# Optimization experiments

Hardware: AMD Instinct MI355X
Metric: run time of the kernel (lower is better)

## Reference

```python
import jax, jax.numpy as jnp
import numpy as np

V, E, H, L, S, T = 100000, 256, 512, 50000, 512, 64


def setup_inputs() -> dict:
    key = jax.random.key(0)
    ks = jax.random.split(key, 14)
    s = 0.02
    return {
        "encoder_outputs": jax.random.normal(ks[0], (1, S, H), jnp.float32),
        "enc_h0": jax.random.normal(ks[1], (1, 1, H), jnp.float32),
        "enc_c0": jax.random.normal(ks[2], (1, 1, H), jnp.float32),
        "emb_table": jax.random.normal(ks[3], (V, E), jnp.float32) * s,
        "W_attn": jax.random.normal(ks[4], (H, E), jnp.float32) * s,
        "b_attn": jnp.zeros((H,), jnp.float32),
        "W_ih": jax.random.normal(ks[5], (4 * H, H), jnp.float32) * s,
        "W_hh": jax.random.normal(ks[6], (4 * H, H), jnp.float32) * s,
        "b_ih": jnp.zeros((4 * H,), jnp.float32),
        "b_hh": jnp.zeros((4 * H,), jnp.float32),
        "W_out": jax.random.normal(ks[7], (L, H), jnp.float32) * s,
        "b_out": jnp.zeros((L,), jnp.float32),
        "word_inputs": jax.random.randint(ks[8], (T,), 0, V),
        "labels": jax.random.randint(ks[9], (T,), 0, L),
    }


def reference(encoder_outputs, enc_h0, enc_c0, emb_table, W_attn, b_attn,
              W_ih, W_hh, b_ih, b_hh, W_out, b_out, word_inputs, labels):
    # batch == 1 throughout (matches forward_train); dropout is identity (eval).
    enc = encoder_outputs[0]          # [S, H]
    h0 = enc_h0[0, 0]                 # [H]  (bidirect hidden already flattened to 1x1xH)
    c0 = enc_c0[0, 0]                 # [H]

    def step(carry, xs):
        h, c = carry
        widx, label = xs
        e = emb_table[widx]                               # [E]   embedding lookup
        q = W_attn @ e + b_attn                           # [H]   attn projection (Linear)
        alphas = jax.nn.softmax(enc @ q)                  # [S]   bmm + softmax
        ctx = alphas @ enc                                # [H]   bmm -> context
        # single-step LSTM (PyTorch gate order: i, f, g, o)
        gates = W_ih @ ctx + b_ih + W_hh @ h + b_hh       # [4H]
        i, f, g, o = jnp.split(gates, 4)
        i = jax.nn.sigmoid(i); f = jax.nn.sigmoid(f)
        g = jnp.tanh(g);       o = jax.nn.sigmoid(o)
        c2 = f * c + i * g
        h2 = o * jnp.tanh(c2)
        logits = W_out @ h2 + b_out                       # [L]   hidden2tag
        ls = jax.nn.log_softmax(logits)
        # NLLLoss(ignore_index=0, reduction='sum')
        step_loss = jnp.where(label == 0, jnp.float32(0.0), -ls[label])
        return (h2, c2), step_loss

    (_, _), losses = jax.lax.scan(step, (h0, c0),
                                  (word_inputs, labels))
    return jnp.sum(losses)
```

## Files before the change

kernel.cpp:

```cpp
#include <hip/hip_runtime.h>
#include <hip/hip_bf16.h>

#define V_ 100000
#define E_ 256
#define H_ 512
#define L_ 50000
#define S_ 512
#define T_ 64
#define NB_ 782
#define NBP_ 784
#define NWG_ 32

typedef short bf16x8 __attribute__((ext_vector_type(8)));
typedef float f32x4 __attribute__((ext_vector_type(4)));

__device__ __forceinline__ float sigm(float x){ return 1.0f/(1.0f+__expf(-x)); }
__device__ __forceinline__ float tanh_fast(float x){
    x = fminf(fmaxf(x, -15.f), 15.f);
    float e = __expf(2.f * x);
    return __fdividef(e - 1.f, e + 1.f);
}
__device__ __forceinline__ unsigned bf16rne(float x){
    unsigned u = __float_as_uint(x);
    return (u + 0x7fffu + ((u >> 16) & 1u)) >> 16;
}
__device__ __forceinline__ float bcast(float v, int l){
    return __uint_as_float(__builtin_amdgcn_readlane(__float_as_uint(v), l));
}

__global__ __launch_bounds__(256) void k_attn(
    const float* __restrict__ enc, const float* __restrict__ emb,
    const float* __restrict__ W_attn, const float* __restrict__ b_attn,
    const int* __restrict__ word_inputs, float* __restrict__ ctx_out)
{
    __shared__ float e_l[E_];
    __shared__ float q_l[H_];
    __shared__ float sc[S_];
    __shared__ float red[8];
    const int t = blockIdx.x, tid = threadIdx.x;
    const int widx = word_inputs[t];

    e_l[tid] = emb[(long)widx * E_ + tid];
    __syncthreads();

    for (int rr = 0; rr < 2; ++rr) {
        int r = tid + rr * 256;
        const float4* wrow = (const float4*)(W_attn + r * E_);
        const float4* ev = (const float4*)e_l;
        float acc = b_attn[r];
        #pragma unroll 8
        for (int j = 0; j < E_ / 4; ++j) {
            float4 w = wrow[j], e4 = ev[j];
            acc += w.x*e4.x + w.y*e4.y + w.z*e4.z + w.w*e4.w;
        }
        q_l[r] = acc;
    }
    __syncthreads();

    for (int rr = 0; rr < 2; ++rr) {
        int s = tid + rr * 256;
        const float4* er = (const float4*)(enc + s * H_);
        const float4* qv = (const float4*)q_l;
        float acc = 0.f;
        #pragma unroll 8
        for (int j = 0; j < H_ / 4; ++j) {
            float4 a = er[j], b = qv[j];
            acc += a.x*b.x + a.y*b.y + a.z*b.z + a.w*b.w;
        }
        sc[s] = acc;
    }
    __syncthreads();

    float m = fmaxf(sc[tid], sc[tid + 256]);
    for (int off = 32; off; off >>= 1) m = fmaxf(m, __shfl_down(m, off));
    if ((tid & 63) == 0) red[tid >> 6] = m;
    __syncthreads();
    if (tid == 0) red[4] = fmaxf(fmaxf(red[0], red[1]), fmaxf(red[2], red[3]));
    __syncthreads();
    m = red[4];
    float e0 = __expf(sc[tid] - m), e1 = __expf(sc[tid + 256] - m);
    sc[tid] = e0; sc[tid + 256] = e1;
    float ssum = e0 + e1;
    for (int off = 32; off; off >>= 1) ssum += __shfl_down(ssum, off);
    if ((tid & 63) == 0) red[tid >> 6] = ssum;
    __syncthreads();
    if (tid == 0) red[5] = red[0] + red[1] + red[2] + red[3];
    __syncthreads();
    float inv = 1.0f / red[5];

    for (int rr = 0; rr < 2; ++rr) {
        int h = tid + rr * 256;
        float acc = 0.f;
        #pragma unroll 4
        for (int s = 0; s < S_; ++s) acc += sc[s] * enc[s * H_ + h];
        ctx_out[t * H_ + h] = acc * inv;
    }
}

__global__ __launch_bounds__(256) void k_gatepre(
    const float* __restrict__ ctx, const float* __restrict__ W_ih,
    const float* __restrict__ b_ih, const float* __restrict__ b_hh,
    float* __restrict__ A_pre)
{
    __shared__ float ctx_t[H_ * 65];
    __shared__ float w_l[8 * H_];
    const int tid = threadIdx.x;
    const int r0 = blockIdx.x * 8;

    for (int i = 0; i < 32; ++i) {
        int p = tid + i * 256;
        int t = p >> 7, k4 = p & 127;
        float4 v = ((const float4*)ctx)[p];
        ctx_t[(k4*4+0)*65 + t] = v.x;
        ctx_t[(k4*4+1)*65 + t] = v.y;
        ctx_t[(k4*4+2)*65 + t] = v.z;
        ctx_t[(k4*4+3)*65 + t] = v.w;
    }
    for (int i = 0; i < 4; ++i) {
        int p = tid + i * 256;
        int row = p >> 7, k4 = p & 127;
        float4 v = ((const float4*)W_ih)[(r0 + row) * (H_/4) + k4];
        float* dst = &w_l[row * H_ + k4 * 4];
        dst[0]=v.x; dst[1]=v.y; dst[2]=v.z; dst[3]=v.w;
    }
    __syncthreads();

    const int t = tid & 63, half = tid >> 6;
    const float* w0 = &w_l[(half*2+0) * H_];
    const float* w1 = &w_l[(half*2+1) * H_];
    float acc0 = 0.f, acc1 = 0.f;
    #pragma unroll 4
    for (int k = 0; k < H_; ++k) {
        float cv = ctx_t[k * 65 + t];
        acc0 += w0[k] * cv;
        acc1 += w1[k] * cv;
    }
    int ra = r0 + half * 2, rb = ra + 1;
    A_pre[t * 2048 + ra] = acc0 + b_ih[ra] + b_hh[ra];
    A_pre[t * 2048 + rb] = acc1 + b_ih[rb] + b_hh[rb];
}

#define ST(i, val) asm volatile("v_accvgpr_write_b32 %0, %1" : "=a"(g##i) : "v"(val));
#define STQ(q,i0,i1,i2,i3) { float4 v_ = wsrc[q]; ST(i0,v_.x) ST(i1,v_.y) ST(i2,v_.z) ST(i3,v_.w) }
#define RD1(i) float wv##i; asm volatile("v_accvgpr_read_b32 %0, %1" : "=v"(wv##i) : "a"(g##i));
#define RD4(i0,i1,i2,i3) RD1(i0) RD1(i1) RD1(i2) RD1(i3)
#define FMA4(i0,i1,i2,i3) \
    a0 += wv##i0 * bcast(hv, i0); a1 += wv##i1 * bcast(hv, i1); \
    a2 += wv##i2 * bcast(hv, i2); a3 += wv##i3 * bcast(hv, i3);

__global__ __launch_bounds__(512, 1) void k_lstm(
    const float* __restrict__ W_hh, const float* __restrict__ A_pre,
    const float* __restrict__ h0, const float* __restrict__ c0,
    float* __restrict__ h_buf)
{
    const int tid = threadIdx.x, wg = blockIdx.x;

    __shared__ float A_l[T_ * 64];
    __shared__ float red[2][8][64];

    const int base = wg * 16;
    const int lane = tid & 63;
    const int ks   = tid >> 6;
    const int G = ((lane >> 4) << 9) + base + (lane & 15);

    float g0,g1,g2,g3,g4,g5,g6,g7,g8,g9,g10,g11,g12,g13,g14,g15;
    float g16,g17,g18,g19,g20,g21,g22,g23,g24,g25,g26,g27,g28,g29,g30,g31;
    float g32,g33,g34,g35,g36,g37,g38,g39,g40,g41,g42,g43,g44,g45,g46,g47;
    float g48,g49,g50,g51,g52,g53,g54,g55,g56,g57,g58,g59,g60,g61,g62,g63;
    {
        const float4* wsrc = (const float4*)(W_hh + (long)G * H_ + ks * 64);
        STQ(0,0,1,2,3)     STQ(1,4,5,6,7)     STQ(2,8,9,10,11)   STQ(3,12,13,14,15)
        STQ(4,16,17,18,19) STQ(5,20,21,22,23) STQ(6,24,25,26,27) STQ(7,28,29,30,31)
        STQ(8,32,33,34,35) STQ(9,36,37,38,39) STQ(10,40,41,42,43)STQ(11,44,45,46,47)
        STQ(12,48,49,50,51)STQ(13,52,53,54,55)STQ(14,56,57,58,59)STQ(15,60,61,62,63)
    }

    for (int i = 0; i < 8; ++i) {
        int p = tid + i * 512;
        int tt = p >> 6, rr = p & 63;
        A_l[p] = A_pre[tt * 2048 + ((rr >> 4) << 9) + base + (rr & 15)];
    }
    float c_reg = 0.f;
    if (tid < 16) c_reg = c0[base + tid];
    __syncthreads();

    const unsigned SENT = 0xFFFFFFFFu;

    for (int t = 0; t < T_; ++t) {
        RD4(0,1,2,3)     RD4(4,5,6,7)     RD4(8,9,10,11)   RD4(12,13,14,15)
        RD4(16,17,18,19) RD4(20,21,22,23) RD4(24,25,26,27) RD4(28,29,30,31)
        RD4(32,33,34,35) RD4(36,37,38,39) RD4(40,41,42,43) RD4(44,45,46,47)
        RD4(48,49,50,51) RD4(52,53,54,55) RD4(56,57,58,59) RD4(60,61,62,63)
        __builtin_amdgcn_sched_barrier(0);

        float hv;
        if (t == 0) {
            hv = h0[ks * 64 + lane];
        } else {
            const unsigned* hb = (const unsigned*)h_buf + (t - 1) * H_ + ks * 64;
            unsigned u = __hip_atomic_load(hb + lane, __ATOMIC_RELAXED,
                                           __HIP_MEMORY_SCOPE_AGENT);
            while (u == SENT) {
                __builtin_amdgcn_s_sleep(1);
                u = __hip_atomic_load(hb + lane, __ATOMIC_RELAXED,
                                      __HIP_MEMORY_SCOPE_AGENT);
            }
            hv = __uint_as_float(u);
        }

        float a0 = 0.f, a1 = 0.f, a2 = 0.f, a3 = 0.f;
        FMA4(0,1,2,3)     FMA4(4,5,6,7)     FMA4(8,9,10,11)   FMA4(12,13,14,15)
        FMA4(16,17,18,19) FMA4(20,21,22,23) FMA4(24,25,26,27) FMA4(28,29,30,31)
        FMA4(32,33,34,35) FMA4(36,37,38,39) FMA4(40,41,42,43) FMA4(44,45,46,47)
        FMA4(48,49,50,51) FMA4(52,53,54,55) FMA4(56,57,58,59) FMA4(60,61,62,63)
        red[t & 1][ks][lane] = (a0 + a1) + (a2 + a3);
        __syncthreads();

        if (ks == 0) {
            float s = A_l[t * 64 + lane];
            #pragma unroll
            for (int k2 = 0; k2 < 8; ++k2) s += red[t & 1][k2][lane];
            float gf_ = __shfl_down(s, 16);
            float gg_ = __shfl_down(s, 32);
            float go_ = __shfl_down(s, 48);
            if (lane < 16) {
                float gi = sigm(s);
                float gf = sigm(gf_);
                float gg = tanh_fast(gg_);
                float go = sigm(go_);
                float c2 = gf * c_reg + gi * gg;
                c_reg = c2;
                float h2 = go * tanh_fast(c2);
                __hip_atomic_store((unsigned*)h_buf + t * H_ + base + lane,
                                   __float_as_uint(h2),
                                   __ATOMIC_RELAXED, __HIP_MEMORY_SCOPE_AGENT);
            }
        }
    }
}

__global__ __launch_bounds__(256) void k_out(
    const float* __restrict__ W_out, const float* __restrict__ b_out,
    const float* __restrict__ h_buf, const int* __restrict__ labels,
    float* __restrict__ pm, float* __restrict__ ps, float* __restrict__ ll)
{
    __shared__ __align__(16) unsigned char smem[65536];
    const int tid = threadIdx.x;
    const int r0 = blockIdx.x * 64;
    const int lane = tid & 63, w = tid >> 6;
    const int g = lane >> 4, li = lane & 15;

    for (int i = 0; i < 32; ++i) {
        int p = tid + i * 256;
        int t = p >> 7, k4 = p & 127;
        float4 v = ((const float4*)h_buf)[p];
        unsigned p01 = bf16rne(v.x) | (bf16rne(v.y) << 16);
        unsigned p23 = bf16rne(v.z) | (bf16rne(v.w) << 16);
        unsigned byte = (unsigned)(t * 1024 + k4 * 8) ^ ((unsigned)(t & 7) << 4);
        *(uint2*)(smem + byte) = make_uint2(p01, p23);
    }

    f32x4 acc0 = {0.f,0.f,0.f,0.f}, acc1 = {0.f,0.f,0.f,0.f};
    f32x4 acc2 = {0.f,0.f,0.f,0.f}, acc3 = {0.f,0.f,0.f,0.f};
    __syncthreads();

    int rrow = r0 + w * 16 + li;
    int rw = rrow < L_ ? rrow : (L_ - 1);
    const float* ap = W_out + (long)rw * H_ + g * 8;

    #pragma unroll
    for (int kk = 0; kk < 16; ++kk) {
        float4 va = *(const float4*)(ap + kk * 32);
        float4 vb = *(const float4*)(ap + kk * 32 + 4);
        union { unsigned u[4]; bf16x8 v; } A;
        A.u[0] = bf16rne(va.x) | (bf16rne(va.y) << 16);
        A.u[1] = bf16rne(va.z) | (bf16rne(va.w) << 16);
        A.u[2] = bf16rne(vb.x) | (bf16rne(vb.y) << 16);
        A.u[3] = bf16rne(vb.z) | (bf16rne(vb.w) << 16);

        #pragma unroll
        for (int nt = 0; nt < 4; ++nt) {
            int t = nt * 16 + li;
            unsigned byte = (unsigned)(t * 1024 + kk * 64 + g * 16)
                          ^ ((unsigned)(t & 7) << 4);
            bf16x8 B = *(const bf16x8*)(smem + byte);
            f32x4* accp = (nt == 0) ? &acc0 : (nt == 1) ? &acc1
                        : (nt == 2) ? &acc2 : &acc3;
            *accp = __builtin_amdgcn_mfma_f32_16x16x32_bf16(A.v, B, *accp, 0, 0, 0);
        }
    }
    __syncthreads();

    float* lg   = (float*)smem;
    float* redb = (float*)(smem + 64 * 65 * 4);
    float* gmax = redb + 256;

    #pragma unroll
    for (int nt = 0; nt < 4; ++nt) {
        const f32x4 a = (nt == 0) ? acc0 : (nt == 1) ? acc1
                      : (nt == 2) ? acc2 : acc3;
        int t = nt * 16 + li;
        #pragma unroll
        for (int q = 0; q < 4; ++q) {
            int rloc = w * 16 + g * 4 + q;
            int r = r0 + rloc;
            float v = -1e30f;
            if (r < L_) v = a[q] + b_out[r];
            lg[rloc * 65 + t] = v;
        }
    }
    __syncthreads();

    const int t = tid & 63, part = tid >> 6;
    float m = -1e30f;
    #pragma unroll
    for (int r16 = 0; r16 < 16; ++r16)
        m = fmaxf(m, lg[(part*16 + r16)*65 + t]);
    redb[part*64 + t] = m;
    __syncthreads();
    if (part == 0)
        gmax[t] = fmaxf(fmaxf(redb[t], redb[64+t]), fmaxf(redb[128+t], redb[192+t]));
    __syncthreads();
    float gm = gmax[t];
    float s = 0.f;
    #pragma unroll
    for (int r16 = 0; r16 < 16; ++r16)
        s += __expf(lg[(part*16 + r16)*65 + t] - gm);
    __syncthreads();
    redb[part*64 + t] = s;
    __syncthreads();
    if (part == 0) {
        pm[t * NBP_ + blockIdx.x] = gm;
        ps[t * NBP_ + blockIdx.x] = redb[t] + redb[64+t] + redb[128+t] + redb[192+t];
        int lb = labels[t];
        if (lb >= r0 && lb < r0 + 64) ll[t] = lg[(lb - r0)*65 + t];
    }
}

__global__ __launch_bounds__(256) void k_final(
    const float* __restrict__ pm, const float* __restrict__ ps,
    const float* __restrict__ ll, const int* __restrict__ labels,
    float* __restrict__ out)
{
    __shared__ float rbuf[8];
    const int t = blockIdx.x, tid = threadIdx.x;
    float m = -1e30f;
    for (int b = tid; b < NB_; b += 256) m = fmaxf(m, pm[t * NBP_ + b]);
    for (int off = 32; off; off >>= 1) m = fmaxf(m, __shfl_down(m, off));
    if ((tid & 63) == 0) rbuf[tid >> 6] = m;
    __syncthreads();
    if (tid == 0) rbuf[4] = fmaxf(fmaxf(rbuf[0], rbuf[1]), fmaxf(rbuf[2], rbuf[3]));
    __syncthreads();
    float M = rbuf[4];
    __syncthreads();
    float s = 0.f;
    for (int b = tid; b < NB_; b += 256)
        s += ps[t * NBP_ + b] * __expf(pm[t * NBP_ + b] - M);
    for (int off = 32; off; off >>= 1) s += __shfl_down(s, off);
    if ((tid & 63) == 0) rbuf[tid >> 6] = s;
    __syncthreads();
    if (tid == 0) {
        float S = rbuf[0] + rbuf[1] + rbuf[2] + rbuf[3];
        int lb = labels[t];
        if (lb != 0) {
            float loss = -(ll[t] - M - __logf(S));
            atomicAdd(out, loss);
        }
    }
}

extern "C" void kernel_launch(void* const* d_in, const int* in_sizes, int n_in,
                              void* d_out, int out_size, void* d_ws, size_t ws_size,
                              hipStream_t stream)
{
    (void)in_sizes; (void)n_in; (void)out_size; (void)ws_size;
    const float* enc    = (const float*)d_in[0];
    const float* h0     = (const float*)d_in[1];
    const float* c0     = (const float*)d_in[2];
    const float* emb    = (const float*)d_in[3];
    const float* W_attn = (const float*)d_in[4];
    const float* b_attn = (const float*)d_in[5];
    const float* W_ih   = (const float*)d_in[6];
    const float* W_hh   = (const float*)d_in[7];
    const float* b_ih   = (const float*)d_in[8];
    const float* b_hh   = (const float*)d_in[9];
    const float* W_out  = (const float*)d_in[10];
    const float* b_out  = (const float*)d_in[11];
    const int* widx     = (const int*)d_in[12];
    const int* labels   = (const int*)d_in[13];
    float* out = (float*)d_out;

    char* ws = (char*)d_ws;
    float* ctx   = (float*)(ws + 0);
    float* A_pre = (float*)(ws + 131072);
    float* h_buf = (float*)(ws + 655360);
    float* pm    = (float*)(ws + 786688);
    float* ps    = (float*)(ws + 987392);
    float* ll    = (float*)(ws + 1188096);

    hipMemsetAsync(h_buf, 0xFF, T_ * H_ * sizeof(float), stream);
    hipMemsetAsync(out, 0, sizeof(float), stream);

    k_attn<<<T_, 256, 0, stream>>>(enc, emb, W_attn, b_attn, widx, ctx);
    k_gatepre<<<256, 256, 0, stream>>>(ctx, W_ih, b_ih, b_hh, A_pre);
    k_lstm<<<NWG_, 512, 0, stream>>>(W_hh, A_pre, h0, c0, h_buf);
    k_out<<<NB_, 256, 0, stream>>>(W_out, b_out, h_buf, labels, pm, ps, ll);
    k_final<<<T_, 256, 0, stream>>>(pm, ps, ll, labels, out);
}
```

Before: 240.1 us.

## Convert W_out to bf16 on idle CUs during the LSTM recurrence

Extra workgroups are added to the latency-bound LSTM launch. They convert W_out from fp32 to bf16 into the workspace while the 32 recurrence workgroups run, and the LSTM also writes h in bf16. A new output kernel reads the pre-converted bf16 weights and h directly from global memory, which halves the bytes it streams and removes the per-tile conversion and shared-memory staging. The risk is that the converter blocks contend for bandwidth and CUs with the recurrence, and the path only runs when the workspace holds about 52 MB.

```diff
diff --git a/kernel.cpp b/kernel.cpp
--- a/kernel.cpp
+++ b/kernel.cpp
@@ -10,6 +10,7 @@
 #define NB_ 782
 #define NBP_ 784
 #define NWG_ 32
+#define NCV_ 224
 
 typedef short bf16x8 __attribute__((ext_vector_type(8)));
 typedef float f32x4 __attribute__((ext_vector_type(4)));
@@ -151,9 +152,26 @@
 __global__ __launch_bounds__(512, 1) void k_lstm(
     const float* __restrict__ W_hh, const float* __restrict__ A_pre,
     const float* __restrict__ h0, const float* __restrict__ c0,
-    float* __restrict__ h_buf)
-{
-    const int tid = threadIdx.x, wg = blockIdx.x;
+    float* __restrict__ h_buf, unsigned short* __restrict__ h_bf,
+    unsigned short* __restrict__ w_bf, const float* __restrict__ W_out)
+{
+    const int tid = threadIdx.x, bid = blockIdx.x;
+
+    if (bid >= NWG_) {
+        const int cid = bid - NWG_;
+        const long total4 = (long)L_ * H_ / 4;
+        const long stride = (long)NCV_ * 512;
+        const float4* src = (const float4*)W_out;
+        uint2* dst = (uint2*)w_bf;
+        for (long i = (long)cid * 512 + tid; i < total4; i += stride) {
+            float4 v = src[i];
+            unsigned lo = bf16rne(v.x) | (bf16rne(v.y) << 16);
+            unsigned hi = bf16rne(v.z) | (bf16rne(v.w) << 16);
+            dst[i] = make_uint2(lo, hi);
+        }
+        return;
+    }
+    const int wg = bid;
 
     __shared__ float A_l[T_ * 64];
     __shared__ float red[2][8][64];
@@ -234,66 +252,45 @@
                 __hip_atomic_store((unsigned*)h_buf + t * H_ + base + lane,
                                    __float_as_uint(h2),
                                    __ATOMIC_RELAXED, __HIP_MEMORY_SCOPE_AGENT);
+                h_bf[t * H_ + base + lane] = (unsigned short)bf16rne(h2);
             }
         }
     }
 }
 
-__global__ __launch_bounds__(256) void k_out(
-    const float* __restrict__ W_out, const float* __restrict__ b_out,
-    const float* __restrict__ h_buf, const int* __restrict__ labels,
+__global__ __launch_bounds__(256) void k_out_bf(
+    const unsigned short* __restrict__ w_bf, const float* __restrict__ b_out,
+    const unsigned short* __restrict__ h_bf, const int* __restrict__ labels,
     float* __restrict__ pm, float* __restrict__ ps, float* __restrict__ ll)
 {
-    __shared__ __align__(16) unsigned char smem[65536];
+    __shared__ float lg[64 * 65];
+    __shared__ float redb[256];
+    __shared__ float gmax[64];
     const int tid = threadIdx.x;
     const int r0 = blockIdx.x * 64;
     const int lane = tid & 63, w = tid >> 6;
     const int g = lane >> 4, li = lane & 15;
 
-    for (int i = 0; i < 32; ++i) {
-        int p = tid + i * 256;
-        int t = p >> 7, k4 = p & 127;
-        float4 v = ((const float4*)h_buf)[p];
-        unsigned p01 = bf16rne(v.x) | (bf16rne(v.y) << 16);
-        unsigned p23 = bf16rne(v.z) | (bf16rne(v.w) << 16);
-        unsigned byte = (unsigned)(t * 1024 + k4 * 8) ^ ((unsigned)(t & 7) << 4);
-        *(uint2*)(smem + byte) = make_uint2(p01, p23);
-    }
-
     f32x4 acc0 = {0.f,0.f,0.f,0.f}, acc1 = {0.f,0.f,0.f,0.f};
     f32x4 acc2 = {0.f,0.f,0.f,0.f}, acc3 = {0.f,0.f,0.f,0.f};
-    __syncthreads();
 
     int rrow = r0 + w * 16 + li;
     int rw = rrow < L_ ? rrow : (L_ - 1);
-    const float* ap = W_out + (long)rw * H_ + g * 8;
+    const bf16x8* ap = (const bf16x8*)(w_bf + (long)rw * H_);
+    const bf16x8* hp = (const bf16x8*)h_bf;
 
     #pragma unroll
     for (int kk = 0; kk < 16; ++kk) {
-        float4 va = *(const float4*)(ap + kk * 32);
-        float4 vb = *(const float4*)(ap + kk * 32 + 4);
-        union { unsigned u[4]; bf16x8 v; } A;
-        A.u[0] = bf16rne(va.x) | (bf16rne(va.y) << 16);
-        A.u[1] = bf16rne(va.z) | (bf16rne(va.w) << 16);
-        A.u[2] = bf16rne(vb.x) | (bf16rne(vb.y) << 16);
-        A.u[3] = bf16rne(vb.z) | (bf16rne(vb.w) << 16);
-
-        #pragma unroll
-        for (int nt = 0; nt < 4; ++nt) {
-            int t = nt * 16 + li;
-            unsigned byte = (unsigned)(t * 1024 + kk * 64 + g * 16)
-                          ^ ((unsigned)(t & 7) << 4);
-            bf16x8 B = *(const bf16x8*)(smem + byte);
-            f32x4* accp = (nt == 0) ? &acc0 : (nt == 1) ? &acc1
-                        : (nt == 2) ? &acc2 : &acc3;
-            *accp = __builtin_amdgcn_mfma_f32_16x16x32_bf16(A.v, B, *accp, 0, 0, 0);
-        }
-    }
-    __syncthreads();
-
-    float* lg   = (float*)smem;
-    float* redb = (float*)(smem + 64 * 65 * 4);
-    float* gmax = redb + 256;
+        bf16x8 A = ap[kk * 4 + g];
+        bf16x8 B0 = hp[(0*16 + li) * 64 + kk*4 + g];
+        bf16x8 B1 = hp[(1*16 + li) * 64 + kk*4 + g];
+        bf16x8 B2 = hp[(2*16 + li) * 64 + kk*4 + g];
+        bf16x8 B3 = hp[(3*16 + li) * 64 + kk*4 + g];
+        acc0 = __builtin_amdgcn_mfma_f32_16x16x32_bf16(A, B0, acc0, 0, 0, 0);
+        acc1 = __builtin_amdgcn_mfma_f32_16x16x32_bf16(A, B1, acc1, 0, 0, 0);
+        acc2 = __builtin_amdgcn_mfma_f32_16x16x32_bf16(A, B2, acc2, 0, 0, 0);
+        acc3 = __builtin_amdgcn_mfma_f32_16x16x32_bf16(A, B3, acc3, 0, 0, 0);
+    }
 
     #pragma unroll
     for (int nt = 0; nt < 4; ++nt) {
@@ -337,6 +334,104 @@
     }
 }
 
+__global__ __launch_bounds__(256) void k_out(
+    const float* __restrict__ W_out, const float* __restrict__ b_out,
+    const float* __restrict__ h_buf, const int* __restrict__ labels,
+    float* __restrict__ pm, float* __restrict__ ps, float* __restrict__ ll)
+{
+    __shared__ __align__(16) unsigned char smem[65536];
+    const int tid = threadIdx.x;
+    const int r0 = blockIdx.x * 64;
+    const int lane = tid & 63, w = tid >> 6;
+    const int g = lane >> 4, li = lane & 15;
+
+    for (int i = 0; i < 32; ++i) {
+        int p = tid + i * 256;
+        int t = p >> 7, k4 = p & 127;
+        float4 v = ((const float4*)h_buf)[p];
+        unsigned p01 = bf16rne(v.x) | (bf16rne(v.y) << 16);
+        unsigned p23 = bf16rne(v.z) | (bf16rne(v.w) << 16);
+        unsigned byte = (unsigned)(t * 1024 + k4 * 8) ^ ((unsigned)(t & 7) << 4);
+        *(uint2*)(smem + byte) = make_uint2(p01, p23);
+    }
+
+    f32x4 acc0 = {0.f,0.f,0.f,0.f}, acc1 = {0.f,0.f,0.f,0.f};
+    f32x4 acc2 = {0.f,0.f,0.f,0.f}, acc3 = {0.f,0.f,0.f,0.f};
+    __syncthreads();
+
+    int rrow = r0 + w * 16 + li;
+    int rw = rrow < L_ ? rrow : (L_ - 1);
+    const float* ap = W_out + (long)rw * H_ + g * 8;
+
+    #pragma unroll
+    for (int kk = 0; kk < 16; ++kk) {
+        float4 va = *(const float4*)(ap + kk * 32);
+        float4 vb = *(const float4*)(ap + kk * 32 + 4);
+        union { unsigned u[4]; bf16x8 v; } A;
+        A.u[0] = bf16rne(va.x) | (bf16rne(va.y) << 16);
+        A.u[1] = bf16rne(va.z) | (bf16rne(va.w) << 16);
+        A.u[2] = bf16rne(vb.x) | (bf16rne(vb.y) << 16);
+        A.u[3] = bf16rne(vb.z) | (bf16rne(vb.w) << 16);
+
+        #pragma unroll
+        for (int nt = 0; nt < 4; ++nt) {
+            int t = nt * 16 + li;
+            unsigned byte = (unsigned)(t * 1024 + kk * 64 + g * 16)
+                          ^ ((unsigned)(t & 7) << 4);
+            bf16x8 B = *(const bf16x8*)(smem + byte);
+            f32x4* accp = (nt == 0) ? &acc0 : (nt == 1) ? &acc1
+                        : (nt == 2) ? &acc2 : &acc3;
+            *accp = __builtin_amdgcn_mfma_f32_16x16x32_bf16(A.v, B, *accp, 0, 0, 0);
+        }
+    }
+    __syncthreads();
+
+    float* lg   = (float*)smem;
+    float* redb = (float*)(smem + 64 * 65 * 4);
+    float* gmax = redb + 256;
+
+    #pragma unroll
+    for (int nt = 0; nt < 4; ++nt) {
+        const f32x4 a = (nt == 0) ? acc0 : (nt == 1) ? acc1
+                      : (nt == 2) ? acc2 : acc3;
+        int t = nt * 16 + li;
+        #pragma unroll
+        for (int q = 0; q < 4; ++q) {
+            int rloc = w * 16 + g * 4 + q;
+            int r = r0 + rloc;
+            float v = -1e30f;
+            if (r < L_) v = a[q] + b_out[r];
+            lg[rloc * 65 + t] = v;
+        }
+    }
+    __syncthreads();
+
+    const int t = tid & 63, part = tid >> 6;
+    float m = -1e30f;
+    #pragma unroll
+    for (int r16 = 0; r16 < 16; ++r16)
+        m = fmaxf(m, lg[(part*16 + r16)*65 + t]);
+    redb[part*64 + t] = m;
+    __syncthreads();
+    if (part == 0)
+        gmax[t] = fmaxf(fmaxf(redb[t], redb[64+t]), fmaxf(redb[128+t], redb[192+t]));
+    __syncthreads();
+    float gm = gmax[t];
+    float s = 0.f;
+    #pragma unroll
+    for (int r16 = 0; r16 < 16; ++r16)
+        s += __expf(lg[(part*16 + r16)*65 + t] - gm);
+    __syncthreads();
+    redb[part*64 + t] = s;
+    __syncthreads();
+    if (part == 0) {
+        pm[t * NBP_ + blockIdx.x] = gm;
+        ps[t * NBP_ + blockIdx.x] = redb[t] + redb[64+t] + redb[128+t] + redb[192+t];
+        int lb = labels[t];
+        if (lb >= r0 && lb < r0 + 64) ll[t] = lg[(lb - r0)*65 + t];
+    }
+}
+
 __global__ __launch_bounds__(256) void k_final(
     const float* __restrict__ pm, const float* __restrict__ ps,
     const float* __restrict__ ll, const int* __restrict__ labels,
@@ -373,7 +468,7 @@
                               void* d_out, int out_size, void* d_ws, size_t ws_size,
                               hipStream_t stream)
 {
-    (void)in_sizes; (void)n_in; (void)out_size; (void)ws_size;
+    (void)in_sizes; (void)n_in; (void)out_size;
     const float* enc    = (const float*)d_in[0];
     const float* h0     = (const float*)d_in[1];
     const float* c0     = (const float*)d_in[2];
@@ -391,19 +486,30 @@
     float* out = (float*)d_out;
 
     char* ws = (char*)d_ws;
-    float* ctx   = (float*)(ws + 0);
-    float* A_pre = (float*)(ws + 131072);
-    float* h_buf = (float*)(ws + 655360);
-    float* pm    = (float*)(ws + 786688);
-    float* ps    = (float*)(ws + 987392);
-    float* ll    = (float*)(ws + 1188096);
+    float* ctx            = (float*)(ws + 0);
+    float* A_pre          = (float*)(ws + 131072);
+    float* h_buf          = (float*)(ws + 655360);
+    float* pm             = (float*)(ws + 786688);
+    float* ps             = (float*)(ws + 987392);
+    float* ll             = (float*)(ws + 1188096);
+    unsigned short* h_bf  = (unsigned short*)(ws + 1188352);
+    unsigned short* w_bf  = (unsigned short*)(ws + 1253888);
+
+    const bool fast = ws_size >= (size_t)52453888;
 
     hipMemsetAsync(h_buf, 0xFF, T_ * H_ * sizeof(float), stream);
     hipMemsetAsync(out, 0, sizeof(float), stream);
 
     k_attn<<<T_, 256, 0, stream>>>(enc, emb, W_attn, b_attn, widx, ctx);
     k_gatepre<<<256, 256, 0, stream>>>(ctx, W_ih, b_ih, b_hh, A_pre);
-    k_lstm<<<NWG_, 512, 0, stream>>>(W_hh, A_pre, h0, c0, h_buf);
-    k_out<<<NB_, 256, 0, stream>>>(W_out, b_out, h_buf, labels, pm, ps, ll);
+    if (fast) {
+        k_lstm<<<NWG_ + NCV_, 512, 0, stream>>>(W_hh, A_pre, h0, c0,
+                                                h_buf, h_bf, w_bf, W_out);
+        k_out_bf<<<NB_, 256, 0, stream>>>(w_bf, b_out, h_bf, labels, pm, ps, ll);
+    } else {
+        k_lstm<<<NWG_, 512, 0, stream>>>(W_hh, A_pre, h0, c0,
+                                         h_buf, h_bf, h_bf , W_out);
+        k_out<<<NB_, 256, 0, stream>>>(W_out, b_out, h_buf, labels, pm, ps, ll);
+    }
     k_final<<<T_, 256, 0, stream>>>(pm, ps, ll, labels, out);
 }
```

New measurement: 260.2 us. 1.08x slower.

## Fuse attention and input-gate projection into the persistent LSTM kernel

Applied to the files above, without the earlier changes.

Merges the attention kernel and the W_ih gate-precompute kernel into the persistent LSTM kernel. Each of the 32 workgroups computes attention context for two timesteps and publishes it to global memory through sentinel-checked atomics. It then holds its W_ih slice in AGPRs and computes its own gate pre-activations before running the recurrence. This removes two kernel launches and the A_pre round trip through global memory. In exchange it doubles AGPR pressure, concentrates attention work on only 32 workgroups, and makes every workgroup spin-wait on contexts produced by the others.

```diff
diff --git a/kernel.cpp b/kernel.cpp
--- a/kernel.cpp
+++ b/kernel.cpp
@@ -28,145 +28,53 @@
     return __uint_as_float(__builtin_amdgcn_readlane(__float_as_uint(v), l));
 }
 
-__global__ __launch_bounds__(256) void k_attn(
-    const float* __restrict__ enc, const float* __restrict__ emb,
-    const float* __restrict__ W_attn, const float* __restrict__ b_attn,
-    const int* __restrict__ word_inputs, float* __restrict__ ctx_out)
-{
-    __shared__ float e_l[E_];
-    __shared__ float q_l[H_];
-    __shared__ float sc[S_];
-    __shared__ float red[8];
-    const int t = blockIdx.x, tid = threadIdx.x;
-    const int widx = word_inputs[t];
-
-    e_l[tid] = emb[(long)widx * E_ + tid];
-    __syncthreads();
-
-    for (int rr = 0; rr < 2; ++rr) {
-        int r = tid + rr * 256;
-        const float4* wrow = (const float4*)(W_attn + r * E_);
-        const float4* ev = (const float4*)e_l;
-        float acc = b_attn[r];
-        #pragma unroll 8
-        for (int j = 0; j < E_ / 4; ++j) {
-            float4 w = wrow[j], e4 = ev[j];
-            acc += w.x*e4.x + w.y*e4.y + w.z*e4.z + w.w*e4.w;
-        }
-        q_l[r] = acc;
-    }
-    __syncthreads();
-
-    for (int rr = 0; rr < 2; ++rr) {
-        int s = tid + rr * 256;
-        const float4* er = (const float4*)(enc + s * H_);
-        const float4* qv = (const float4*)q_l;
-        float acc = 0.f;
-        #pragma unroll 8
-        for (int j = 0; j < H_ / 4; ++j) {
-            float4 a = er[j], b = qv[j];
-            acc += a.x*b.x + a.y*b.y + a.z*b.z + a.w*b.w;
-        }
-        sc[s] = acc;
-    }
-    __syncthreads();
-
-    float m = fmaxf(sc[tid], sc[tid + 256]);
-    for (int off = 32; off; off >>= 1) m = fmaxf(m, __shfl_down(m, off));
-    if ((tid & 63) == 0) red[tid >> 6] = m;
-    __syncthreads();
-    if (tid == 0) red[4] = fmaxf(fmaxf(red[0], red[1]), fmaxf(red[2], red[3]));
-    __syncthreads();
-    m = red[4];
-    float e0 = __expf(sc[tid] - m), e1 = __expf(sc[tid + 256] - m);
-    sc[tid] = e0; sc[tid + 256] = e1;
-    float ssum = e0 + e1;
-    for (int off = 32; off; off >>= 1) ssum += __shfl_down(ssum, off);
-    if ((tid & 63) == 0) red[tid >> 6] = ssum;
-    __syncthreads();
-    if (tid == 0) red[5] = red[0] + red[1] + red[2] + red[3];
-    __syncthreads();
-    float inv = 1.0f / red[5];
-
-    for (int rr = 0; rr < 2; ++rr) {
-        int h = tid + rr * 256;
-        float acc = 0.f;
-        #pragma unroll 4
-        for (int s = 0; s < S_; ++s) acc += sc[s] * enc[s * H_ + h];
-        ctx_out[t * H_ + h] = acc * inv;
-    }
-}
-
-__global__ __launch_bounds__(256) void k_gatepre(
-    const float* __restrict__ ctx, const float* __restrict__ W_ih,
-    const float* __restrict__ b_ih, const float* __restrict__ b_hh,
-    float* __restrict__ A_pre)
-{
-    __shared__ float ctx_t[H_ * 65];
-    __shared__ float w_l[8 * H_];
-    const int tid = threadIdx.x;
-    const int r0 = blockIdx.x * 8;
-
-    for (int i = 0; i < 32; ++i) {
-        int p = tid + i * 256;
-        int t = p >> 7, k4 = p & 127;
-        float4 v = ((const float4*)ctx)[p];
-        ctx_t[(k4*4+0)*65 + t] = v.x;
-        ctx_t[(k4*4+1)*65 + t] = v.y;
-        ctx_t[(k4*4+2)*65 + t] = v.z;
-        ctx_t[(k4*4+3)*65 + t] = v.w;
-    }
-    for (int i = 0; i < 4; ++i) {
-        int p = tid + i * 256;
-        int row = p >> 7, k4 = p & 127;
-        float4 v = ((const float4*)W_ih)[(r0 + row) * (H_/4) + k4];
-        float* dst = &w_l[row * H_ + k4 * 4];
-        dst[0]=v.x; dst[1]=v.y; dst[2]=v.z; dst[3]=v.w;
-    }
-    __syncthreads();
-
-    const int t = tid & 63, half = tid >> 6;
-    const float* w0 = &w_l[(half*2+0) * H_];
-    const float* w1 = &w_l[(half*2+1) * H_];
-    float acc0 = 0.f, acc1 = 0.f;
-    #pragma unroll 4
-    for (int k = 0; k < H_; ++k) {
-        float cv = ctx_t[k * 65 + t];
-        acc0 += w0[k] * cv;
-        acc1 += w1[k] * cv;
-    }
-    int ra = r0 + half * 2, rb = ra + 1;
-    A_pre[t * 2048 + ra] = acc0 + b_ih[ra] + b_hh[ra];
-    A_pre[t * 2048 + rb] = acc1 + b_ih[rb] + b_hh[rb];
-}
-
 #define ST(i, val) asm volatile("v_accvgpr_write_b32 %0, %1" : "=a"(g##i) : "v"(val));
 #define STQ(q,i0,i1,i2,i3) { float4 v_ = wsrc[q]; ST(i0,v_.x) ST(i1,v_.y) ST(i2,v_.z) ST(i3,v_.w) }
+#define STJ(i, val) asm volatile("v_accvgpr_write_b32 %0, %1" : "=a"(j##i) : "v"(val));
+#define STJQ(q,i0,i1,i2,i3) { float4 v_ = wsrc2[q]; STJ(i0,v_.x) STJ(i1,v_.y) STJ(i2,v_.z) STJ(i3,v_.w) }
 #define RD1(i) float wv##i; asm volatile("v_accvgpr_read_b32 %0, %1" : "=v"(wv##i) : "a"(g##i));
 #define RD4(i0,i1,i2,i3) RD1(i0) RD1(i1) RD1(i2) RD1(i3)
 #define FMA4(i0,i1,i2,i3) \
     a0 += wv##i0 * bcast(hv, i0); a1 += wv##i1 * bcast(hv, i1); \
     a2 += wv##i2 * bcast(hv, i2); a3 += wv##i3 * bcast(hv, i3);
-
-__global__ __launch_bounds__(512, 1) void k_lstm(
-    const float* __restrict__ W_hh, const float* __restrict__ A_pre,
+#define MJ4(i0,i1,i2,i3) { float w0_,w1_,w2_,w3_; \
+  asm volatile("v_accvgpr_read_b32 %0, %1" : "=v"(w0_) : "a"(j##i0)); \
+  asm volatile("v_accvgpr_read_b32 %0, %1" : "=v"(w1_) : "a"(j##i1)); \
+  asm volatile("v_accvgpr_read_b32 %0, %1" : "=v"(w2_) : "a"(j##i2)); \
+  asm volatile("v_accvgpr_read_b32 %0, %1" : "=v"(w3_) : "a"(j##i3)); \
+  a0 += w0_ * bcast(cv, i0); a1 += w1_ * bcast(cv, i1); \
+  a2 += w2_ * bcast(cv, i2); a3 += w3_ * bcast(cv, i3); }
+
+__global__ __launch_bounds__(512, 1) void k_fused(
+    const float* __restrict__ enc, const float* __restrict__ emb,
+    const float* __restrict__ W_attn, const float* __restrict__ b_attn,
+    const int* __restrict__ word_inputs,
+    const float* __restrict__ W_ih, const float* __restrict__ b_ih,
+    const float* __restrict__ b_hh, const float* __restrict__ W_hh,
     const float* __restrict__ h0, const float* __restrict__ c0,
-    float* __restrict__ h_buf)
+    float* __restrict__ ctx_g, float* __restrict__ h_buf)
 {
-    const int tid = threadIdx.x, wg = blockIdx.x;
-
     __shared__ float A_l[T_ * 64];
     __shared__ float red[2][8][64];
-
-    const int base = wg * 16;
+    __shared__ float e_l2[512];
+    __shared__ float q_l2[1024];
+    __shared__ float sc2[1024];
+    __shared__ float red8[16];
+
+    const int tid = threadIdx.x, wg = blockIdx.x;
     const int lane = tid & 63;
     const int ks   = tid >> 6;
+    const int base = wg * 16;
     const int G = ((lane >> 4) << 9) + base + (lane & 15);
 
     float g0,g1,g2,g3,g4,g5,g6,g7,g8,g9,g10,g11,g12,g13,g14,g15;
     float g16,g17,g18,g19,g20,g21,g22,g23,g24,g25,g26,g27,g28,g29,g30,g31;
     float g32,g33,g34,g35,g36,g37,g38,g39,g40,g41,g42,g43,g44,g45,g46,g47;
     float g48,g49,g50,g51,g52,g53,g54,g55,g56,g57,g58,g59,g60,g61,g62,g63;
+    float j0,j1,j2,j3,j4,j5,j6,j7,j8,j9,j10,j11,j12,j13,j14,j15;
+    float j16,j17,j18,j19,j20,j21,j22,j23,j24,j25,j26,j27,j28,j29,j30,j31;
+    float j32,j33,j34,j35,j36,j37,j38,j39,j40,j41,j42,j43,j44,j45,j46,j47;
+    float j48,j49,j50,j51,j52,j53,j54,j55,j56,j57,j58,j59,j60,j61,j62,j63;
     {
         const float4* wsrc = (const float4*)(W_hh + (long)G * H_ + ks * 64);
         STQ(0,0,1,2,3)     STQ(1,4,5,6,7)     STQ(2,8,9,10,11)   STQ(3,12,13,14,15)
@@ -174,17 +82,123 @@
         STQ(8,32,33,34,35) STQ(9,36,37,38,39) STQ(10,40,41,42,43)STQ(11,44,45,46,47)
         STQ(12,48,49,50,51)STQ(13,52,53,54,55)STQ(14,56,57,58,59)STQ(15,60,61,62,63)
     }
-
-    for (int i = 0; i < 8; ++i) {
-        int p = tid + i * 512;
-        int tt = p >> 6, rr = p & 63;
-        A_l[p] = A_pre[tt * 2048 + ((rr >> 4) << 9) + base + (rr & 15)];
-    }
+    {
+        const float4* wsrc2 = (const float4*)(W_ih + (long)G * H_ + ks * 64);
+        STJQ(0,0,1,2,3)     STJQ(1,4,5,6,7)     STJQ(2,8,9,10,11)   STJQ(3,12,13,14,15)
+        STJQ(4,16,17,18,19) STJQ(5,20,21,22,23) STJQ(6,24,25,26,27) STJQ(7,28,29,30,31)
+        STJQ(8,32,33,34,35) STJQ(9,36,37,38,39) STJQ(10,40,41,42,43)STJQ(11,44,45,46,47)
+        STJQ(12,48,49,50,51)STJQ(13,52,53,54,55)STJQ(14,56,57,58,59)STJQ(15,60,61,62,63)
+    }
+
     float c_reg = 0.f;
     if (tid < 16) c_reg = c0[base + tid];
-    __syncthreads();
+    float bb = 0.f;
+    if (tid < 64) bb = b_ih[G] + b_hh[G];
 
     const unsigned SENT = 0xFFFFFFFFu;
+
+    {
+        const int t0 = wg * 2, t1 = wg * 2 + 1;
+        const int w0i = word_inputs[t0], w1i = word_inputs[t1];
+        if (tid < 256) e_l2[tid] = emb[(long)w0i * E_ + tid];
+        else           e_l2[tid] = emb[(long)w1i * E_ + (tid - 256)];
+        __syncthreads();
+
+        {
+            const float4* wrow = (const float4*)(W_attn + tid * E_);
+            const float4* e0p = (const float4*)e_l2;
+            const float4* e1p = (const float4*)(e_l2 + 256);
+            float acc0 = b_attn[tid], acc1 = acc0;
+            #pragma unroll 8
+            for (int j2 = 0; j2 < E_ / 4; ++j2) {
+                float4 w = wrow[j2], a = e0p[j2], b = e1p[j2];
+                acc0 += w.x*a.x + w.y*a.y + w.z*a.z + w.w*a.w;
+                acc1 += w.x*b.x + w.y*b.y + w.z*b.z + w.w*b.w;
+            }
+            q_l2[tid] = acc0; q_l2[512 + tid] = acc1;
+        }
+        __syncthreads();
+
+        float acc0 = 0.f, acc1 = 0.f;
+        {
+            const float4* er = (const float4*)(enc + tid * H_);
+            const float4* q0p = (const float4*)q_l2;
+            const float4* q1p = (const float4*)(q_l2 + 512);
+            #pragma unroll 8
+            for (int j2 = 0; j2 < H_ / 4; ++j2) {
+                float4 e = er[j2], a = q0p[j2], b = q1p[j2];
+                acc0 += e.x*a.x + e.y*a.y + e.z*a.z + e.w*a.w;
+                acc1 += e.x*b.x + e.y*b.y + e.z*b.z + e.w*b.w;
+            }
+        }
+        float m0 = acc0, m1 = acc1;
+        for (int off = 32; off; off >>= 1) {
+            m0 = fmaxf(m0, __shfl_down(m0, off));
+            m1 = fmaxf(m1, __shfl_down(m1, off));
+        }
+        if (lane == 0) { red8[ks] = m0; red8[8 + ks] = m1; }
+        __syncthreads();
+        float M0 = red8[0], M1 = red8[8];
+        #pragma unroll
+        for (int i2 = 1; i2 < 8; ++i2) {
+            M0 = fmaxf(M0, red8[i2]); M1 = fmaxf(M1, red8[8 + i2]);
+        }
+        float e0v = __expf(acc0 - M0), e1v = __expf(acc1 - M1);
+        sc2[tid] = e0v; sc2[512 + tid] = e1v;
+        float s0 = e0v, s1 = e1v;
+        for (int off = 32; off; off >>= 1) {
+            s0 += __shfl_down(s0, off);
+            s1 += __shfl_down(s1, off);
+        }
+        __syncthreads();
+        if (lane == 0) { red8[ks] = s0; red8[8 + ks] = s1; }
+        __syncthreads();
+        float S0 = 0.f, S1 = 0.f;
+        #pragma unroll
+        for (int i2 = 0; i2 < 8; ++i2) { S0 += red8[i2]; S1 += red8[8 + i2]; }
+        float inv0 = 1.f / S0, inv1 = 1.f / S1;
+
+        float c0a = 0.f, c1a = 0.f;
+        #pragma unroll 4
+        for (int s = 0; s < S_; ++s) {
+            float ev = enc[s * H_ + tid];
+            c0a += sc2[s] * ev;
+            c1a += sc2[512 + s] * ev;
+        }
+        c0a *= inv0; c1a *= inv1;
+        __hip_atomic_store((unsigned*)ctx_g + t0 * H_ + tid, __float_as_uint(c0a),
+                           __ATOMIC_RELAXED, __HIP_MEMORY_SCOPE_AGENT);
+        __hip_atomic_store((unsigned*)ctx_g + t1 * H_ + tid, __float_as_uint(c1a),
+                           __ATOMIC_RELAXED, __HIP_MEMORY_SCOPE_AGENT);
+    }
+
+    for (int t = 0; t < T_; ++t) {
+        float cv;
+        {
+            const unsigned* cb = (const unsigned*)ctx_g + t * H_ + ks * 64;
+            unsigned u = __hip_atomic_load(cb + lane, __ATOMIC_RELAXED,
+                                           __HIP_MEMORY_SCOPE_AGENT);
+            while (u == SENT) {
+                __builtin_amdgcn_s_sleep(1);
+                u = __hip_atomic_load(cb + lane, __ATOMIC_RELAXED,
+                                      __HIP_MEMORY_SCOPE_AGENT);
+            }
+            cv = __uint_as_float(u);
+        }
+        float a0 = 0.f, a1 = 0.f, a2 = 0.f, a3 = 0.f;
+        MJ4(0,1,2,3)     MJ4(4,5,6,7)     MJ4(8,9,10,11)   MJ4(12,13,14,15)
+        MJ4(16,17,18,19) MJ4(20,21,22,23) MJ4(24,25,26,27) MJ4(28,29,30,31)
+        MJ4(32,33,34,35) MJ4(36,37,38,39) MJ4(40,41,42,43) MJ4(44,45,46,47)
+        MJ4(48,49,50,51) MJ4(52,53,54,55) MJ4(56,57,58,59) MJ4(60,61,62,63)
+        red[t & 1][ks][lane] = (a0 + a1) + (a2 + a3);
+        __syncthreads();
+        if (ks == 0) {
+            float s = bb;
+            #pragma unroll
+            for (int k2 = 0; k2 < 8; ++k2) s += red[t & 1][k2][lane];
+            A_l[t * 64 + lane] = s;
+        }
+    }
 
     for (int t = 0; t < T_; ++t) {
         RD4(0,1,2,3)     RD4(4,5,6,7)     RD4(8,9,10,11)   RD4(12,13,14,15)
@@ -391,19 +405,18 @@
     float* out = (float*)d_out;
 
     char* ws = (char*)d_ws;
-    float* ctx   = (float*)(ws + 0);
-    float* A_pre = (float*)(ws + 131072);
-    float* h_buf = (float*)(ws + 655360);
-    float* pm    = (float*)(ws + 786688);
-    float* ps    = (float*)(ws + 987392);
-    float* ll    = (float*)(ws + 1188096);
-
-    hipMemsetAsync(h_buf, 0xFF, T_ * H_ * sizeof(float), stream);
+    float* h_buf = (float*)(ws + 0);
+    float* ctx_g = (float*)(ws + 131072);
+    float* pm    = (float*)(ws + 262144);
+    float* ps    = (float*)(ws + 462848);
+    float* ll    = (float*)(ws + 663552);
+
+    hipMemsetAsync(h_buf, 0xFF, 2 * T_ * H_ * sizeof(float), stream);
     hipMemsetAsync(out, 0, sizeof(float), stream);
 
-    k_attn<<<T_, 256, 0, stream>>>(enc, emb, W_attn, b_attn, widx, ctx);
-    k_gatepre<<<256, 256, 0, stream>>>(ctx, W_ih, b_ih, b_hh, A_pre);
-    k_lstm<<<NWG_, 512, 0, stream>>>(W_hh, A_pre, h0, c0, h_buf);
+    k_fused<<<NWG_, 512, 0, stream>>>(enc, emb, W_attn, b_attn, widx,
+                                      W_ih, b_ih, b_hh, W_hh, h0, c0,
+                                      ctx_g, h_buf);
     k_out<<<NB_, 256, 0, stream>>>(W_out, b_out, h_buf, labels, pm, ps, ll);
     k_final<<<T_, 256, 0, stream>>>(pm, ps, ll, labels, out);
 }
```

Result: slower. 270.9 us (+12.8%).

## Rewrite attention kernel with wave-cooperative coalesced row dot products

Applied to the files above, without the earlier changes.

The attention kernel moves from one-thread-per-row dot products to one-wave-per-row dot products. Each lane reads a contiguous float4 slice of the W_attn or encoder row, and the partial sums are combined with xor shuffles. The aim is to replace strided, uncoalesced per-thread row reads with coalesced loads. The block size also doubles to 512 so the context reduction needs one column per thread. The cost is added shuffle reductions for every row.

```diff
diff --git a/kernel.cpp b/kernel.cpp
--- a/kernel.cpp
+++ b/kernel.cpp
@@ -28,7 +28,7 @@
     return __uint_as_float(__builtin_amdgcn_readlane(__float_as_uint(v), l));
 }
 
-__global__ __launch_bounds__(256) void k_attn(
+__global__ __launch_bounds__(512) void k_attn2(
     const float* __restrict__ enc, const float* __restrict__ emb,
     const float* __restrict__ W_attn, const float* __restrict__ b_attn,
     const int* __restrict__ word_inputs, float* __restrict__ ctx_out)
@@ -36,65 +36,73 @@
     __shared__ float e_l[E_];
     __shared__ float q_l[H_];
     __shared__ float sc[S_];
-    __shared__ float red[8];
+    __shared__ float red8[8];
     const int t = blockIdx.x, tid = threadIdx.x;
+    const int lane = tid & 63, wv = tid >> 6;
     const int widx = word_inputs[t];
 
-    e_l[tid] = emb[(long)widx * E_ + tid];
-    __syncthreads();
-
-    for (int rr = 0; rr < 2; ++rr) {
-        int r = tid + rr * 256;
-        const float4* wrow = (const float4*)(W_attn + r * E_);
-        const float4* ev = (const float4*)e_l;
-        float acc = b_attn[r];
-        #pragma unroll 8
-        for (int j = 0; j < E_ / 4; ++j) {
-            float4 w = wrow[j], e4 = ev[j];
-            acc += w.x*e4.x + w.y*e4.y + w.z*e4.z + w.w*e4.w;
-        }
-        q_l[r] = acc;
-    }
-    __syncthreads();
-
-    for (int rr = 0; rr < 2; ++rr) {
-        int s = tid + rr * 256;
-        const float4* er = (const float4*)(enc + s * H_);
-        const float4* qv = (const float4*)q_l;
-        float acc = 0.f;
-        #pragma unroll 8
-        for (int j = 0; j < H_ / 4; ++j) {
-            float4 a = er[j], b = qv[j];
-            acc += a.x*b.x + a.y*b.y + a.z*b.z + a.w*b.w;
-        }
-        sc[s] = acc;
-    }
-    __syncthreads();
-
-    float m = fmaxf(sc[tid], sc[tid + 256]);
-    for (int off = 32; off; off >>= 1) m = fmaxf(m, __shfl_down(m, off));
-    if ((tid & 63) == 0) red[tid >> 6] = m;
-    __syncthreads();
-    if (tid == 0) red[4] = fmaxf(fmaxf(red[0], red[1]), fmaxf(red[2], red[3]));
-    __syncthreads();
-    m = red[4];
-    float e0 = __expf(sc[tid] - m), e1 = __expf(sc[tid + 256] - m);
-    sc[tid] = e0; sc[tid + 256] = e1;
-    float ssum = e0 + e1;
-    for (int off = 32; off; off >>= 1) ssum += __shfl_down(ssum, off);
-    if ((tid & 63) == 0) red[tid >> 6] = ssum;
-    __syncthreads();
-    if (tid == 0) red[5] = red[0] + red[1] + red[2] + red[3];
-    __syncthreads();
-    float inv = 1.0f / red[5];
-
-    for (int rr = 0; rr < 2; ++rr) {
-        int h = tid + rr * 256;
-        float acc = 0.f;
-        #pragma unroll 4
-        for (int s = 0; s < S_; ++s) acc += sc[s] * enc[s * H_ + h];
-        ctx_out[t * H_ + h] = acc * inv;
-    }
+    if (tid < E_) e_l[tid] = emb[(long)widx * E_ + tid];
+    __syncthreads();
+
+    {
+        float4 e4 = *(const float4*)(e_l + lane * 4);
+        float b_pre = b_attn[wv * 64 + lane];
+        #pragma unroll 2
+        for (int i = 0; i < 64; ++i) {
+            int r = wv * 64 + i;
+            float4 w = *(const float4*)(W_attn + (long)r * E_ + lane * 4);
+            float p = w.x*e4.x + w.y*e4.y + w.z*e4.z + w.w*e4.w;
+            #pragma unroll
+            for (int off = 32; off; off >>= 1) p += __shfl_xor(p, off);
+            if (lane == i) q_l[r] = p + b_pre;
+        }
+    }
+    __syncthreads();
+
+    {
+        float4 qa = *(const float4*)(q_l + lane * 8);
+        float4 qb = *(const float4*)(q_l + lane * 8 + 4);
+        #pragma unroll 2
+        for (int i = 0; i < 64; ++i) {
+            int s = wv * 64 + i;
+            const float* er = enc + (long)s * H_ + lane * 8;
+            float4 ea = *(const float4*)er;
+            float4 eb = *(const float4*)(er + 4);
+            float p = ea.x*qa.x + ea.y*qa.y + ea.z*qa.z + ea.w*qa.w
+                    + eb.x*qb.x + eb.y*qb.y + eb.z*qb.z + eb.w*qb.w;
+            #pragma unroll
+            for (int off = 32; off; off >>= 1) p += __shfl_xor(p, off);
+            if (lane == i) sc[s] = p;
+        }
+    }
+    __syncthreads();
+
+    float v = sc[tid];
+    float m = v;
+    #pragma unroll
+    for (int off = 32; off; off >>= 1) m = fmaxf(m, __shfl_xor(m, off));
+    if (lane == 0) red8[wv] = m;
+    __syncthreads();
+    float M = red8[0];
+    #pragma unroll
+    for (int i = 1; i < 8; ++i) M = fmaxf(M, red8[i]);
+    float ev = __expf(v - M);
+    float ssum = ev;
+    #pragma unroll
+    for (int off = 32; off; off >>= 1) ssum += __shfl_xor(ssum, off);
+    __syncthreads();
+    sc[tid] = ev;
+    if (lane == 0) red8[wv] = ssum;
+    __syncthreads();
+    float S = 0.f;
+    #pragma unroll
+    for (int i = 0; i < 8; ++i) S += red8[i];
+    float inv = 1.0f / S;
+
+    float acc = 0.f;
+    #pragma unroll 4
+    for (int s = 0; s < S_; ++s) acc += sc[s] * enc[s * H_ + tid];
+    ctx_out[t * H_ + tid] = acc * inv;
 }
 
 __global__ __launch_bounds__(256) void k_gatepre(
@@ -401,7 +409,7 @@
     hipMemsetAsync(h_buf, 0xFF, T_ * H_ * sizeof(float), stream);
     hipMemsetAsync(out, 0, sizeof(float), stream);
 
-    k_attn<<<T_, 256, 0, stream>>>(enc, emb, W_attn, b_attn, widx, ctx);
+    k_attn2<<<T_, 512, 0, stream>>>(enc, emb, W_attn, b_attn, widx, ctx);
     k_gatepre<<<256, 256, 0, stream>>>(ctx, W_ih, b_ih, b_hh, A_pre);
     k_lstm<<<NWG_, 512, 0, stream>>>(W_hh, A_pre, h0, c0, h_buf);
     k_out<<<NB_, 256, 0, stream>>>(W_out, b_out, h_buf, labels, pm, ps, ll);
```

After: 238.8 us. No clear change (-0.6%).
